# Kernel optimization log

Hardware: AMD Instinct MI355X
Metric: run time of the kernel (lower is better)

## Reference

```python
import jax, jax.numpy as jnp
import numpy as np

DIM = 384
HEADS = 12
CUBE = (4, 7, 7)
N = CUBE[0] * CUBE[1] * CUBE[2]  # 196
HIDDEN = 4 * DIM
BW = 256  # num_windows * batch
EPS = 1e-5


def _relative_position_index():
    c, h, w = CUBE
    coords = np.stack(np.meshgrid(np.arange(c), np.arange(h), np.arange(w), indexing='ij'))  # [3,c,h,w]
    flat = coords.reshape(3, -1)  # [3, N]
    rel = flat[:, :, None] - flat[:, None, :]  # [3, N, N]
    rel = rel.transpose(1, 2, 0).copy()
    rel[:, :, 0] += c - 1
    rel[:, :, 1] += h - 1
    rel[:, :, 2] += w - 1
    rel[:, :, 1] *= 2 * w - 1
    rel[:, :, 0] *= (2 * h - 1) * (2 * w - 1)
    return rel.sum(-1).astype(np.int32)  # [N, N]


def setup_inputs() -> dict:
    key = jax.random.key(0)
    ks = jax.random.split(key, 16)
    s = 0.02
    table_rows = (2 * CUBE[0] - 1) * (2 * CUBE[1] - 1) * (2 * CUBE[2] - 1)
    return {
        'x': jax.random.normal(ks[0], (BW, N, DIM), jnp.float32),
        'norm1_w': jnp.ones((DIM,), jnp.float32),
        'norm1_b': jnp.zeros((DIM,), jnp.float32),
        'qkv_w': jax.random.normal(ks[1], (DIM, 3 * DIM), jnp.float32) * s,
        'qkv_b': jnp.zeros((3 * DIM,), jnp.float32),
        'proj_w': jax.random.normal(ks[2], (DIM, DIM), jnp.float32) * s,
        'proj_b': jnp.zeros((DIM,), jnp.float32),
        'rpb_table': jax.random.normal(ks[3], (table_rows, HEADS), jnp.float32) * s,
        'norm2_w': jnp.ones((DIM,), jnp.float32),
        'norm2_b': jnp.zeros((DIM,), jnp.float32),
        'fc1_w': jax.random.normal(ks[4], (DIM, HIDDEN), jnp.float32) * s,
        'fc1_b': jnp.zeros((HIDDEN,), jnp.float32),
        'fc2_w': jax.random.normal(ks[5], (HIDDEN, DIM), jnp.float32) * s,
        'fc2_b': jnp.zeros((DIM,), jnp.float32),
        'rpi': jnp.asarray(_relative_position_index()),
    }


def _layernorm(x, w, b):
    mu = jnp.mean(x, axis=-1, keepdims=True)
    var = jnp.mean(jnp.square(x - mu), axis=-1, keepdims=True)
    return (x - mu) * jax.lax.rsqrt(var + EPS) * w + b


def reference(x, norm1_w, norm1_b, qkv_w, qkv_b, proj_w, proj_b, rpb_table,
              norm2_w, norm2_b, fc1_w, fc1_b, fc2_w, fc2_b, rpi):
    B_, n, C = x.shape
    hd = C // HEADS
    scale = hd ** (-0.5)

    # --- attention branch ---
    h = _layernorm(x, norm1_w, norm1_b)
    qkv = (h @ qkv_w + qkv_b).reshape(B_, n, 3, HEADS, hd)
    q, k, v = qkv[:, :, 0], qkv[:, :, 1], qkv[:, :, 2]  # [B_, n, H, hd]
    attn = jnp.einsum('bqhd,bkhd->bhqk', q * scale, k)
    bias = rpb_table[rpi]                 # [n, n, H]
    attn = attn + jnp.transpose(bias, (2, 0, 1))[None]
    attn = jax.nn.softmax(attn, axis=-1)
    out = jnp.einsum('bhqk,bkhd->bqhd', attn, v).reshape(B_, n, C)
    out = out @ proj_w + proj_b
    x = x + out

    # --- MLP branch ---
    h = _layernorm(x, norm2_w, norm2_b)
    h = jax.nn.gelu(h @ fc1_w + fc1_b, approximate=False)
    h = h @ fc2_w + fc2_b
    return x + h
```

## Files before the change

kernel.cpp:

```cpp
#include <hip/hip_runtime.h>
#include <hip/hip_bf16.h>
#include <math.h>

#define NDIM 384
#define NHEADS 12
#define NTOK 196
#define NBATCH 256
#define M_TOK (NBATCH * NTOK)
#define NHID 1536
#define THREE_DIM 1152
#define HD 32
#define EPSV 1e-5f
#define BH_STRIDE 7168
#define BPAD 224

typedef __hip_bfloat16 bf16;
typedef __attribute__((ext_vector_type(8))) short short8;
typedef __attribute__((ext_vector_type(4))) short short4v;
typedef __attribute__((ext_vector_type(4))) float f32x4;

__device__ __forceinline__ void gload_lds16(const void* g, void* l) {
  __builtin_amdgcn_global_load_lds((const __attribute__((address_space(1))) void*)g,
                                   (__attribute__((address_space(3))) void*)l, 16, 0, 0);
}

__global__ void k_transpose_bf16(const float* __restrict__ src, bf16* __restrict__ dst,
                                 int K, int N) {
  int idx = blockIdx.x * 256 + threadIdx.x;
  if (idx >= K * N) return;
  int k = idx / N, n = idx - k * N;
  dst[n * K + k] = __float2bfloat16(src[idx]);
}

__global__ void k_build_bias(const float* __restrict__ table, const int* __restrict__ rpi,
                             float* __restrict__ bias_pad) {
  int idx = blockIdx.x * 256 + threadIdx.x;
  if (idx >= NHEADS * BPAD * BPAD) return;
  int h = idx / (BPAD * BPAD);
  int rem = idx - h * (BPAD * BPAD);
  int r = rem / BPAD, c = rem - r * BPAD;
  float v;
  if (c >= NTOK) {
    v = -1e30f;
  } else {
    int rr = r < NTOK ? r : NTOK - 1;
    v = table[rpi[rr * NTOK + c] * NHEADS + h];
  }
  bias_pad[idx] = v;
}

__global__ __launch_bounds__(256) void k_layernorm(const float* __restrict__ x,
                                                   const float* __restrict__ w,
                                                   const float* __restrict__ b,
                                                   bf16* __restrict__ out) {
  int token = blockIdx.x * 4 + (threadIdx.x >> 6);
  int lane = threadIdx.x & 63;
  const float* xr = x + (size_t)token * NDIM;
  float v[6];
  float s = 0.f;
#pragma unroll
  for (int i = 0; i < 6; ++i) { v[i] = xr[lane + i * 64]; s += v[i]; }
#pragma unroll
  for (int off = 32; off >= 1; off >>= 1) s += __shfl_xor(s, off);
  float mu = s * (1.f / NDIM);
  float s2 = 0.f;
#pragma unroll
  for (int i = 0; i < 6; ++i) { float d = v[i] - mu; s2 += d * d; }
#pragma unroll
  for (int off = 32; off >= 1; off >>= 1) s2 += __shfl_xor(s2, off);
  float r = rsqrtf(s2 * (1.f / NDIM) + EPSV);
  bf16* orow = out + (size_t)token * NDIM;
#pragma unroll
  for (int i = 0; i < 6; ++i) {
    int c = lane + i * 64;
    orow[c] = __float2bfloat16((v[i] - mu) * r * w[c] + b[c]);
  }
}

template <int EPI>
__global__ __launch_bounds__(256) void k_gemm_bt(const bf16* __restrict__ A,
                                                 const bf16* __restrict__ Bt,
                                                 const float* __restrict__ bias,
                                                 const float* __restrict__ resid,
                                                 void* __restrict__ Cout,
                                                 bf16* __restrict__ pq,
                                                 bf16* __restrict__ pk,
                                                 bf16* __restrict__ pv,
                                                 int Nn, int K, int nbx) {
  __shared__ bf16 As[2][128 * 32];
  __shared__ bf16 Bs[2][128 * 32];
  const int tid = threadIdx.x;
  const int wave = tid >> 6, lane = tid & 63;
  const int lo = lane & 15, hi = lane >> 4;
  const int wm = wave >> 1, wn = wave & 1;

  const int nwg = gridDim.x;
  const int swz = (blockIdx.x & 7) * (nwg >> 3) + (blockIdx.x >> 3);
  const int m0 = (swz / nbx) * 128, n0 = (swz % nbx) * 128;

  f32x4 acc[4][4];
#pragma unroll
  for (int i = 0; i < 4; ++i) {
#pragma unroll
    for (int j = 0; j < 4; ++j) acc[i][j] = (f32x4){0.f, 0.f, 0.f, 0.f};
  }

  const int row = tid >> 2, part = tid & 3;
  const int row1 = (256 + tid) >> 2, part1 = tid & 3;

  gload_lds16(A + (size_t)(m0 + row) * K + part * 8, As[0] + tid * 8);
  gload_lds16(Bt + (size_t)(n0 + row) * K + part * 8, Bs[0] + tid * 8);
  gload_lds16(A + (size_t)(m0 + row1) * K + part1 * 8, As[0] + (256 + tid) * 8);
  gload_lds16(Bt + (size_t)(n0 + row1) * K + part1 * 8, Bs[0] + (256 + tid) * 8);
  __syncthreads();

  const int nk = K >> 5;
  int cur = 0;
  for (int ks = 0; ks < nk; ++ks) {
    if (ks + 1 < nk) {
      int k0 = (ks + 1) << 5;
      gload_lds16(A + (size_t)(m0 + row) * K + k0 + part * 8, As[cur ^ 1] + tid * 8);
      gload_lds16(Bt + (size_t)(n0 + row) * K + k0 + part * 8, Bs[cur ^ 1] + tid * 8);
      gload_lds16(A + (size_t)(m0 + row1) * K + k0 + part1 * 8, As[cur ^ 1] + (256 + tid) * 8);
      gload_lds16(Bt + (size_t)(n0 + row1) * K + k0 + part1 * 8, Bs[cur ^ 1] + (256 + tid) * 8);
    }
    short8 af[4], bfr[4];
#pragma unroll
    for (int i = 0; i < 4; ++i) {
      af[i] = *(const short8*)(As[cur] + (wm * 64 + i * 16 + lo) * 32 + hi * 8);
      bfr[i] = *(const short8*)(Bs[cur] + (wn * 64 + i * 16 + lo) * 32 + hi * 8);
    }
#pragma unroll
    for (int i = 0; i < 4; ++i) {
#pragma unroll
      for (int j = 0; j < 4; ++j)
        acc[i][j] = __builtin_amdgcn_mfma_f32_16x16x32_bf16(af[i], bfr[j], acc[i][j], 0, 0, 0);
    }
    __syncthreads();
    cur ^= 1;
  }

  const float qscale = 0.17677669529663687f;
#pragma unroll
  for (int i = 0; i < 4; ++i) {
    int rbase = m0 + wm * 64 + i * 16 + hi * 4;
#pragma unroll
    for (int j = 0; j < 4; ++j) {
      int cb = n0 + wn * 64 + j * 16 + lo;
      float bv = bias[cb];
      if (EPI == 3) {
        int d = cb & 31;
        int hseg = cb >> 5;
        int which = hseg / 12;
        int h = hseg - which * 12;
        int b = rbase / 196;
        int t0 = rbase - b * 196;
        size_t base = (size_t)(b * 12 + h) * BH_STRIDE;
        if (which == 2) {
          union { short4v v; bf16 x[4]; } pack;
#pragma unroll
          for (int e = 0; e < 4; ++e) pack.x[e] = __float2bfloat16(acc[i][j][e] + bv);
          *(short4v*)(pv + base + d * BPAD + t0) = pack.v;
        } else if (which == 1) {
#pragma unroll
          for (int e = 0; e < 4; ++e)
            pk[base + (t0 + e) * 32 + d] = __float2bfloat16(acc[i][j][e] + bv);
        } else {
#pragma unroll
          for (int e = 0; e < 4; ++e)
            pq[base + (t0 + e) * 32 + d] = __float2bfloat16((acc[i][j][e] + bv) * qscale);
        }
      } else {
#pragma unroll
        for (int e = 0; e < 4; ++e) {
          int rr = rbase + e;
          float val = acc[i][j][e] + bv;
          if (EPI == 1) val = 0.5f * val * (1.f + erff(val * 0.70710678118f));
          if (EPI == 2) {
            size_t idx = (size_t)rr * Nn + cb;
            ((float*)Cout)[idx] = resid[idx] + val;
          } else {
            size_t idx = (size_t)rr * Nn + cb;
            ((bf16*)Cout)[idx] = __float2bfloat16(val);
          }
        }
      }
    }
  }
}

__global__ __launch_bounds__(256) void k_attn(const bf16* __restrict__ Qp,
                                              const bf16* __restrict__ Kp,
                                              const bf16* __restrict__ Vtp,
                                              const float* __restrict__ bias_pad,
                                              bf16* __restrict__ out) {
  __shared__ __align__(16) bf16 Ps[4][16][232];
  const int tid = threadIdx.x;
  const int wave = tid >> 6, lane = tid & 63;
  const int lo = lane & 15, hi = lane >> 4;
  const int nwg = gridDim.x;
  const int swz = (blockIdx.x & 7) * (nwg >> 3) + (blockIdx.x >> 3);
  const int unit = swz * 4 + wave;
  const int bh = unit / 13;
  const int qt = unit - bh * 13;
  const int h = bh % 12;
  const int b = bh / 12;
  const bf16* Qb = Qp + (size_t)bh * BH_STRIDE;
  const bf16* Kb = Kp + (size_t)bh * BH_STRIDE;
  const bf16* Vb = Vtp + (size_t)bh * BH_STRIDE;

  for (int i = lane; i < 256; i += 64)
    Ps[wave][i >> 4][208 + (i & 15)] = __float2bfloat16(0.f);

  short8 qf = *(const short8*)(Qb + (qt * 16 + lo) * 32 + hi * 8);

  f32x4 s[13];
  __builtin_amdgcn_s_setprio(1);
#pragma unroll
  for (int kt = 0; kt < 13; ++kt) {
    short8 kf = *(const short8*)(Kb + (kt * 16 + lo) * 32 + hi * 8);
    f32x4 z = {0.f, 0.f, 0.f, 0.f};
    s[kt] = __builtin_amdgcn_mfma_f32_16x16x32_bf16(qf, kf, z, 0, 0, 0);
  }
  __builtin_amdgcn_s_setprio(0);

#pragma unroll
  for (int e = 0; e < 4; ++e) {
    int qg = qt * 16 + hi * 4 + e;
    const float* brow = bias_pad + ((size_t)h * BPAD + qg) * BPAD;
    float mx = -1e30f;
#pragma unroll
    for (int kt = 0; kt < 13; ++kt) {
      float v = s[kt][e] + brow[kt * 16 + lo];
      s[kt][e] = v;
      mx = fmaxf(mx, v);
    }
#pragma unroll
    for (int off = 8; off >= 1; off >>= 1) mx = fmaxf(mx, __shfl_xor(mx, off));
    float sm = 0.f;
#pragma unroll
    for (int kt = 0; kt < 13; ++kt) {
      float pe = __expf(s[kt][e] - mx);
      s[kt][e] = pe;
      sm += pe;
    }
#pragma unroll
    for (int off = 8; off >= 1; off >>= 1) sm += __shfl_xor(sm, off);
    float inv = 1.f / sm;
#pragma unroll
    for (int kt = 0; kt < 13; ++kt) s[kt][e] *= inv;
  }

#pragma unroll
  for (int kt = 0; kt < 13; ++kt) {
#pragma unroll
    for (int e = 0; e < 4; ++e)
      Ps[wave][hi * 4 + e][kt * 16 + lo] = __float2bfloat16(s[kt][e]);
  }

  f32x4 o[2] = {{0.f, 0.f, 0.f, 0.f}, {0.f, 0.f, 0.f, 0.f}};
  __builtin_amdgcn_s_setprio(1);
#pragma unroll
  for (int c = 0; c < 7; ++c) {
    short8 pa = *(const short8*)(&Ps[wave][lo][c * 32 + hi * 8]);
#pragma unroll
    for (int n = 0; n < 2; ++n) {
      short8 vf = *(const short8*)(Vb + (n * 16 + lo) * BPAD + c * 32 + hi * 8);
      o[n] = __builtin_amdgcn_mfma_f32_16x16x32_bf16(pa, vf, o[n], 0, 0, 0);
    }
  }
  __builtin_amdgcn_s_setprio(0);

#pragma unroll
  for (int n = 0; n < 2; ++n) {
#pragma unroll
    for (int e = 0; e < 4; ++e) {
      int qg = qt * 16 + hi * 4 + e;
      if (qg < NTOK)
        out[(size_t)(b * NTOK + qg) * NDIM + h * HD + n * 16 + lo] = __float2bfloat16(o[n][e]);
    }
  }
}

extern "C" void kernel_launch(void* const* d_in, const int* in_sizes, int n_in,
                              void* d_out, int out_size, void* d_ws, size_t ws_size,
                              hipStream_t stream) {
  const float* x       = (const float*)d_in[0];
  const float* norm1_w = (const float*)d_in[1];
  const float* norm1_b = (const float*)d_in[2];
  const float* qkv_w   = (const float*)d_in[3];
  const float* qkv_b   = (const float*)d_in[4];
  const float* proj_w  = (const float*)d_in[5];
  const float* proj_b  = (const float*)d_in[6];
  const float* rpb     = (const float*)d_in[7];
  const float* norm2_w = (const float*)d_in[8];
  const float* norm2_b = (const float*)d_in[9];
  const float* fc1_w   = (const float*)d_in[10];
  const float* fc1_b   = (const float*)d_in[11];
  const float* fc2_w   = (const float*)d_in[12];
  const float* fc2_b   = (const float*)d_in[13];
  const int*   rpi     = (const int*)d_in[14];
  float* out = (float*)d_out;

  char* ws = (char*)d_ws;
  bf16* pad_q = (bf16*)ws;
  bf16* pad_k = (bf16*)(ws + 44040192);
  bf16* pad_v = (bf16*)(ws + 2 * 44040192);
  float* bias_pad = (float*)(ws + 3 * 44040192);
  bf16* mlp1 = (bf16*)ws;
  bf16* hbuf = (bf16*)(ws + 154140672);
  bf16* wqkv_t = (bf16*)(ws + 154140672 + 38535168);
  bf16* wproj_t = wqkv_t + 442368;
  bf16* wfc1_t = wproj_t + 147456;
  bf16* wfc2_t = wfc1_t + 589824;

  k_transpose_bf16<<<(442368 + 255) / 256, 256, 0, stream>>>(qkv_w, wqkv_t, 384, 1152);
  k_transpose_bf16<<<(147456 + 255) / 256, 256, 0, stream>>>(proj_w, wproj_t, 384, 384);
  k_transpose_bf16<<<(589824 + 255) / 256, 256, 0, stream>>>(fc1_w, wfc1_t, 384, 1536);
  k_transpose_bf16<<<(589824 + 255) / 256, 256, 0, stream>>>(fc2_w, wfc2_t, 1536, 384);
  k_build_bias<<<(NHEADS * BPAD * BPAD + 255) / 256, 256, 0, stream>>>(rpb, rpi, bias_pad);

  k_layernorm<<<M_TOK / 4, 256, 0, stream>>>(x, norm1_w, norm1_b, hbuf);
  k_gemm_bt<3><<<9 * 392, 256, 0, stream>>>(hbuf, wqkv_t, qkv_b, nullptr, nullptr,
                                            pad_q, pad_k, pad_v, 1152, 384, 9);
  k_attn<<<9984, 256, 0, stream>>>(pad_q, pad_k, pad_v, bias_pad, hbuf);
  k_gemm_bt<2><<<3 * 392, 256, 0, stream>>>(hbuf, wproj_t, proj_b, x, out,
                                            nullptr, nullptr, nullptr, 384, 384, 3);
  k_layernorm<<<M_TOK / 4, 256, 0, stream>>>(out, norm2_w, norm2_b, hbuf);
  k_gemm_bt<1><<<12 * 392, 256, 0, stream>>>(hbuf, wfc1_t, fc1_b, nullptr, mlp1,
                                             nullptr, nullptr, nullptr, 1536, 384, 12);
  k_gemm_bt<2><<<3 * 392, 256, 0, stream>>>(mlp1, wfc2_t, fc2_b, out, out,
                                            nullptr, nullptr, nullptr, 384, 1536, 3);
}
```

Before: 535.3 us.

## Triple-buffer GEMM LDS with XOR swizzle and use tanh-approx GELU

Moves the GEMM mainloop from double to triple buffering of LDS tiles, issuing loads two k-steps ahead and using raw s_waitcnt/s_barrier so more global loads stay in flight across the barrier. Adds an XOR swizzle of the 16-byte chunks within each LDS row to reduce bank conflicts on the fragment reads. It also replaces the exact erf GELU in the fc1 epilogue with the tanh approximation computed via exp and a fast reciprocal. That approximation departs from the reference's exact GELU and could exceed tolerance.

```diff
diff --git a/kernel.cpp b/kernel.cpp
--- a/kernel.cpp
+++ b/kernel.cpp
@@ -87,8 +87,8 @@
                                                  bf16* __restrict__ pk,
                                                  bf16* __restrict__ pv,
                                                  int Nn, int K, int nbx) {
-  __shared__ bf16 As[2][128 * 32];
-  __shared__ bf16 Bs[2][128 * 32];
+  __shared__ __align__(16) bf16 As[3][4096];
+  __shared__ __align__(16) bf16 Bs[3][4096];
   const int tid = threadIdx.x;
   const int wave = tid >> 6, lane = tid & 63;
   const int lo = lane & 15, hi = lane >> 4;
@@ -100,45 +100,59 @@
 
   f32x4 acc[4][4];
 #pragma unroll
-  for (int i = 0; i < 4; ++i) {
+  for (int i = 0; i < 4; ++i)
 #pragma unroll
     for (int j = 0; j < 4; ++j) acc[i][j] = (f32x4){0.f, 0.f, 0.f, 0.f};
-  }
-
-  const int row = tid >> 2, part = tid & 3;
-  const int row1 = (256 + tid) >> 2, part1 = tid & 3;
-
-  gload_lds16(A + (size_t)(m0 + row) * K + part * 8, As[0] + tid * 8);
-  gload_lds16(Bt + (size_t)(n0 + row) * K + part * 8, Bs[0] + tid * 8);
-  gload_lds16(A + (size_t)(m0 + row1) * K + part1 * 8, As[0] + (256 + tid) * 8);
-  gload_lds16(Bt + (size_t)(n0 + row1) * K + part1 * 8, Bs[0] + (256 + tid) * 8);
-  __syncthreads();
+
+  const int row0 = tid >> 2, sw0 = (tid & 3) ^ ((row0 >> 1) & 3);
+  const int c1 = 256 + tid;
+  const int row1 = c1 >> 2, sw1 = (c1 & 3) ^ ((row1 >> 1) & 3);
+  const bf16* Arow0 = A + (size_t)(m0 + row0) * K + sw0 * 8;
+  const bf16* Brow0 = Bt + (size_t)(n0 + row0) * K + sw0 * 8;
+  const bf16* Arow1 = A + (size_t)(m0 + row1) * K + sw1 * 8;
+  const bf16* Brow1 = Bt + (size_t)(n0 + row1) * K + sw1 * 8;
+
+#define STAGE(ks, abuf, bbuf)                                   \
+  {                                                             \
+    int k0_ = (ks) << 5;                                        \
+    gload_lds16(Arow0 + k0_, (abuf) + tid * 8);                 \
+    gload_lds16(Brow0 + k0_, (bbuf) + tid * 8);                 \
+    gload_lds16(Arow1 + k0_, (abuf) + (256 + tid) * 8);         \
+    gload_lds16(Brow1 + k0_, (bbuf) + (256 + tid) * 8);         \
+  }
+
+  bf16* a0 = As[0]; bf16* a1 = As[1]; bf16* a2 = As[2];
+  bf16* b0 = Bs[0]; bf16* b1 = Bs[1]; bf16* b2 = Bs[2];
 
   const int nk = K >> 5;
-  int cur = 0;
+  STAGE(0, a0, b0);
+  STAGE(1, a1, b1);
+  asm volatile("s_waitcnt vmcnt(4)\n\ts_barrier" ::: "memory");
+
+  const int rsw = (lo >> 1) & 3;
   for (int ks = 0; ks < nk; ++ks) {
-    if (ks + 1 < nk) {
-      int k0 = (ks + 1) << 5;
-      gload_lds16(A + (size_t)(m0 + row) * K + k0 + part * 8, As[cur ^ 1] + tid * 8);
-      gload_lds16(Bt + (size_t)(n0 + row) * K + k0 + part * 8, Bs[cur ^ 1] + tid * 8);
-      gload_lds16(A + (size_t)(m0 + row1) * K + k0 + part1 * 8, As[cur ^ 1] + (256 + tid) * 8);
-      gload_lds16(Bt + (size_t)(n0 + row1) * K + k0 + part1 * 8, Bs[cur ^ 1] + (256 + tid) * 8);
-    }
+    if (ks + 2 < nk) STAGE(ks + 2, a2, b2);
     short8 af[4], bfr[4];
 #pragma unroll
     for (int i = 0; i < 4; ++i) {
-      af[i] = *(const short8*)(As[cur] + (wm * 64 + i * 16 + lo) * 32 + hi * 8);
-      bfr[i] = *(const short8*)(Bs[cur] + (wn * 64 + i * 16 + lo) * 32 + hi * 8);
-    }
-#pragma unroll
-    for (int i = 0; i < 4; ++i) {
+      af[i] = *(const short8*)(a0 + (wm * 64 + i * 16 + lo) * 32 + (hi ^ rsw) * 8);
+      bfr[i] = *(const short8*)(b0 + (wn * 64 + i * 16 + lo) * 32 + (hi ^ rsw) * 8);
+    }
+#pragma unroll
+    for (int i = 0; i < 4; ++i)
 #pragma unroll
       for (int j = 0; j < 4; ++j)
         acc[i][j] = __builtin_amdgcn_mfma_f32_16x16x32_bf16(af[i], bfr[j], acc[i][j], 0, 0, 0);
-    }
-    __syncthreads();
-    cur ^= 1;
-  }
+    if (ks + 1 < nk) {
+      if (ks + 2 < nk)
+        asm volatile("s_waitcnt vmcnt(4)\n\ts_barrier" ::: "memory");
+      else
+        asm volatile("s_waitcnt vmcnt(0)\n\ts_barrier" ::: "memory");
+    }
+    bf16* ta = a0; a0 = a1; a1 = a2; a2 = ta;
+    bf16* tb = b0; b0 = b1; b1 = b2; b2 = tb;
+  }
+#undef STAGE
 
   const float qscale = 0.17677669529663687f;
 #pragma unroll
@@ -175,7 +189,13 @@
         for (int e = 0; e < 4; ++e) {
           int rr = rbase + e;
           float val = acc[i][j][e] + bv;
-          if (EPI == 1) val = 0.5f * val * (1.f + erff(val * 0.70710678118f));
+          if (EPI == 1) {
+            float t = val * val;
+            float p = __builtin_fmaf(0.044715f * val, t, val);
+            float E = __expf(1.5957691216057308f * p);
+            float r = __builtin_amdgcn_rcpf(E + 1.f);
+            val = val - val * r;
+          }
           if (EPI == 2) {
             size_t idx = (size_t)rr * Nn + cb;
             ((float*)Cout)[idx] = resid[idx] + val;
```

Result: no change. 537.7 us (+0.4%).
